# Kernel optimization log

Hardware: AMD Instinct MI355X
Metric: run time of the kernel (lower is better)

## Reference

```python
import jax, jax.numpy as jnp
import numpy as np

N = 50000      # nodes
E = 800000     # edges (no self loops; GATConv adds them itself)
F_IN = 128     # in_channels
ED = 16        # edge_attr_dim
H1, C1 = 8, 8  # layer-1 heads/channels -> 64 concat
OUT = 128      # out_channels
G = 256        # graphs in batch
NEG_SLOPE = 0.2


def setup_inputs() -> dict:
    key = jax.random.key(0)
    ks = jax.random.split(key, 20)
    x = jax.random.normal(ks[0], (N, F_IN), jnp.float32)
    src = jax.random.randint(ks[1], (E,), 0, N, jnp.int32)
    off = jax.random.randint(ks[2], (E,), 1, N, jnp.int32)
    dst = ((src + off) % N).astype(jnp.int32)  # guaranteed no self loops
    edge_index = jnp.stack([src, dst])
    edge_attr = jax.random.normal(ks[3], (E, ED), jnp.float32)
    batch = jnp.sort(jax.random.randint(ks[4], (N,), 0, G, jnp.int32))
    def glorot(k, shape, fan_in):
        return jax.random.normal(k, shape, jnp.float32) / np.sqrt(fan_in)
    params = dict(
        W1=glorot(ks[5], (F_IN, H1 * C1), F_IN),
        att_src1=glorot(ks[6], (H1, C1), C1),
        att_dst1=glorot(ks[7], (H1, C1), C1),
        att_edge1=glorot(ks[8], (H1, C1), C1),
        We1=glorot(ks[9], (ED, H1 * C1), ED),
        b1=jnp.zeros((H1 * C1,), jnp.float32),
        W2=glorot(ks[10], (H1 * C1, OUT), H1 * C1),
        att_src2=glorot(ks[11], (1, OUT), OUT),
        att_dst2=glorot(ks[12], (1, OUT), OUT),
        att_edge2=glorot(ks[13], (1, OUT), OUT),
        We2=glorot(ks[14], (ED, OUT), ED),
        b2=jnp.zeros((OUT,), jnp.float32),
    )
    return dict(x=x, edge_index=edge_index, edge_attr=edge_attr, batch=batch, **params)


def _segment_softmax(a, seg, n):
    m = jax.ops.segment_max(a, seg, num_segments=n)
    e = jnp.exp(a - m[seg])
    s = jax.ops.segment_sum(e, seg, num_segments=n)
    return e / (s[seg] + 1e-16)


def _gat_layer(x, src, dst, ea_full, W, a_s, a_d, a_e, We, b, heads, ch, concat):
    n = x.shape[0]
    xw = (x @ W).reshape(n, heads, ch)                       # [N,H,C]
    al_s = jnp.einsum('nhc,hc->nh', xw, a_s)                  # [N,H]
    al_d = jnp.einsum('nhc,hc->nh', xw, a_d)
    ew = (ea_full @ We).reshape(-1, heads, ch)                # [E',H,C]
    al_e = jnp.einsum('ehc,hc->eh', ew, a_e)
    alpha = al_s[src] + al_d[dst] + al_e                      # [E',H]
    alpha = jax.nn.leaky_relu(alpha, NEG_SLOPE)
    alpha = _segment_softmax(alpha, dst, n)                   # softmax over incoming edges
    out = jax.ops.segment_sum(xw[src] * alpha[:, :, None], dst, num_segments=n)
    out = out.reshape(n, heads * ch) if concat else out.mean(axis=1)
    return out + b


def reference(x, edge_index, edge_attr, batch,
              W1, att_src1, att_dst1, att_edge1, We1, b1,
              W2, att_src2, att_dst2, att_edge2, We2, b2):
    src, dst = edge_index[0], edge_index[1]
    n = x.shape[0]
    # add self loops; self-loop edge_attr = mean of incoming edge_attr (fill_value='mean')
    ones = jnp.ones((src.shape[0],), x.dtype)
    deg = jax.ops.segment_sum(ones, dst, num_segments=n)
    ea_self = jax.ops.segment_sum(edge_attr, dst, num_segments=n) / jnp.maximum(deg, 1.0)[:, None]
    loop = jnp.arange(n, dtype=src.dtype)
    src_f = jnp.concatenate([src, loop])
    dst_f = jnp.concatenate([dst, loop])
    ea_full = jnp.concatenate([edge_attr, ea_self], axis=0)

    h = _gat_layer(x, src_f, dst_f, ea_full, W1, att_src1, att_dst1, att_edge1, We1, b1, H1, C1, True)
    h = jax.nn.elu(h)
    h = _gat_layer(h, src_f, dst_f, ea_full, W2, att_src2, att_dst2, att_edge2, We2, b2, 1, OUT, True)

    # global mean pool over graphs
    cnt = jax.ops.segment_sum(jnp.ones((n,), h.dtype), batch, num_segments=G)
    pooled = jax.ops.segment_sum(h, batch, num_segments=G) / jnp.maximum(cnt, 1.0)[:, None]
    return pooled
```

## Files before the change

### kernel.cpp

```cpp
#include <hip/hip_runtime.h>
#include <hip/hip_bf16.h>
#include <math.h>

#define N_NODES 50000
#define N_EDGES 800000
#define F_IN    128
#define ED_DIM  16
#define D1      64
#define NGRAPH  256
#define OUT_C   128

__global__ void prep_kernel(const float* __restrict__ W1, const float* __restrict__ W2,
                            float* __restrict__ W1t, float* __restrict__ W2t) {
  int t = blockIdx.x * 256 + threadIdx.x;
  if (t < 64 * 128) {
    int k = t >> 6, c = t & 63;
    W1t[c * 128 + k] = W1[t];
    int k2 = t >> 7, c2 = t & 127;
    W2t[c2 * 64 + k2] = W2[t];
  }
}

__global__ void hist_kernel(const int* __restrict__ dst, int* __restrict__ deg) {
  int i = blockIdx.x * blockDim.x + threadIdx.x;
  int stride = gridDim.x * blockDim.x;
  for (; i < N_EDGES; i += stride) atomicAdd(&deg[dst[i]], 1);
}

__global__ void scan1_kernel(const int* __restrict__ deg, int* __restrict__ offs,
                             int* __restrict__ bsum) {
  __shared__ int sh[256];
  int b = blockIdx.x, t = threadIdx.x, i = b * 256 + t;
  int v = (i < N_NODES) ? deg[i] : 0;
  sh[t] = v;
  __syncthreads();
  for (int o = 1; o < 256; o <<= 1) {
    int tv = (t >= o) ? sh[t - o] : 0;
    __syncthreads();
    sh[t] += tv;
    __syncthreads();
  }
  if (i < N_NODES) offs[i + 1] = sh[t];
  if (t == 255) bsum[b] = sh[255];
}

__global__ void scan2_kernel(int* __restrict__ bsum) {
  __shared__ int sh[256];
  int t = threadIdx.x;
  sh[t] = (t < 196) ? bsum[t] : 0;
  __syncthreads();
  for (int o = 1; o < 256; o <<= 1) {
    int tv = (t >= o) ? sh[t - o] : 0;
    __syncthreads();
    sh[t] += tv;
    __syncthreads();
  }
  if (t < 196) bsum[t] = (t > 0) ? sh[t - 1] : 0;
}

__global__ void scan3_kernel(const int* __restrict__ bsum, int* __restrict__ offs) {
  int b = blockIdx.x, t = threadIdx.x, i = b * 256 + t;
  if (i < N_NODES) offs[i + 1] += bsum[b];
  if (i == 0) offs[0] = 0;
}

__global__ void scatter_kernel(const int* __restrict__ src, const int* __restrict__ dst,
                               const float* __restrict__ ea,
                               const float* __restrict__ We1, const float* __restrict__ ae1,
                               const float* __restrict__ We2, const float* __restrict__ ae2,
                               const int* __restrict__ offs, int* __restrict__ cnt,
                               int* __restrict__ csr_src,
                               float* __restrict__ al_e1s, float* __restrict__ al_e2s) {
  __shared__ float M1s[16][8];
  __shared__ float M2s[16];
  int t = threadIdx.x;
  if (t < 128) {
    int d = t >> 3, h = t & 7;
    float s = 0.f;
    #pragma unroll
    for (int c = 0; c < 8; ++c) s = fmaf(We1[d * 64 + h * 8 + c], ae1[h * 8 + c], s);
    M1s[d][h] = s;
  } else if (t < 144) {
    int d = t - 128;
    float s = 0.f;
    for (int c = 0; c < 128; ++c) s = fmaf(We2[d * 128 + c], ae2[c], s);
    M2s[d] = s;
  }
  __syncthreads();
  int i = blockIdx.x * blockDim.x + t;
  int stride = gridDim.x * blockDim.x;
  for (; i < N_EDGES; i += stride) {
    int s = src[i], d = dst[i];
    float e[16];
    const float4* ea4 = (const float4*)(ea + (size_t)i * 16);
    #pragma unroll
    for (int q = 0; q < 4; ++q) {
      float4 v = ea4[q];
      e[q * 4] = v.x; e[q * 4 + 1] = v.y; e[q * 4 + 2] = v.z; e[q * 4 + 3] = v.w;
    }
    int pos = offs[d] + atomicAdd(&cnt[d], 1);
    csr_src[pos] = s;
    float r[8];
    #pragma unroll
    for (int h = 0; h < 8; ++h) {
      float sacc = 0.f;
      #pragma unroll
      for (int dd = 0; dd < 16; ++dd) sacc = fmaf(e[dd], M1s[dd][h], sacc);
      r[h] = sacc;
    }
    float4* o4 = (float4*)(al_e1s + (size_t)pos * 8);
    o4[0] = make_float4(r[0], r[1], r[2], r[3]);
    o4[1] = make_float4(r[4], r[5], r[6], r[7]);
    float s2 = 0.f;
    #pragma unroll
    for (int dd = 0; dd < 16; ++dd) s2 = fmaf(e[dd], M2s[dd], s2);
    al_e2s[pos] = s2;
  }
}

__global__ __launch_bounds__(256) void gemm1_kernel(
    const float* __restrict__ x, const float* __restrict__ W1t,
    const float* __restrict__ as1, const float* __restrict__ ad1,
    float* __restrict__ xw1, float* __restrict__ al_s1, float* __restrict__ al_d1) {
  __shared__ float xl[64 * 132];
  __shared__ float wl[64 * 132];
  int t = threadIdx.x;
  int row0 = blockIdx.x * 64;
  const float4* xg = (const float4*)(x + (size_t)row0 * 128);
  const float4* wg = (const float4*)W1t;
  #pragma unroll
  for (int j = 0; j < 8; ++j) {
    int idx = t + j * 256;
    int r = idx >> 5, kq = idx & 31;
    float4 v = make_float4(0.f, 0.f, 0.f, 0.f);
    if (row0 + r < N_NODES) v = xg[r * 32 + kq];
    *(float4*)&xl[r * 132 + kq * 4] = v;
    *(float4*)&wl[(idx >> 5) * 132 + kq * 4] = wg[idx];
  }
  __syncthreads();
  int c0 = t & 15;
  int r4 = (t >> 4) * 4;
  float acc[4][4];
  #pragma unroll
  for (int i = 0; i < 4; ++i)
    #pragma unroll
    for (int j = 0; j < 4; ++j) acc[i][j] = 0.f;
  #pragma unroll 4
  for (int kq = 0; kq < 32; ++kq) {
    float4 xv[4], wv[4];
    #pragma unroll
    for (int i = 0; i < 4; ++i) xv[i] = *(const float4*)&xl[(r4 + i) * 132 + kq * 4];
    #pragma unroll
    for (int j = 0; j < 4; ++j) wv[j] = *(const float4*)&wl[(c0 + 16 * j) * 132 + kq * 4];
    #pragma unroll
    for (int i = 0; i < 4; ++i)
      #pragma unroll
      for (int j = 0; j < 4; ++j) {
        acc[i][j] = fmaf(xv[i].x, wv[j].x, acc[i][j]);
        acc[i][j] = fmaf(xv[i].y, wv[j].y, acc[i][j]);
        acc[i][j] = fmaf(xv[i].z, wv[j].z, acc[i][j]);
        acc[i][j] = fmaf(xv[i].w, wv[j].w, acc[i][j]);
      }
  }
  #pragma unroll
  for (int i = 0; i < 4; ++i) {
    int r = row0 + r4 + i;
    if (r < N_NODES) {
      #pragma unroll
      for (int j = 0; j < 4; ++j) xw1[(size_t)r * 64 + c0 + 16 * j] = acc[i][j];
    }
  }
  float ps[4][4], pd[4][4];
  #pragma unroll
  for (int j = 0; j < 4; ++j) {
    float asv = as1[c0 + 16 * j], adv = ad1[c0 + 16 * j];
    #pragma unroll
    for (int i = 0; i < 4; ++i) { ps[i][j] = acc[i][j] * asv; pd[i][j] = acc[i][j] * adv; }
  }
  #pragma unroll
  for (int m = 1; m <= 4; m <<= 1)
    #pragma unroll
    for (int i = 0; i < 4; ++i)
      #pragma unroll
      for (int j = 0; j < 4; ++j) {
        ps[i][j] += __shfl_xor(ps[i][j], m);
        pd[i][j] += __shfl_xor(pd[i][j], m);
      }
  if ((t & 7) == 0) {
    int half = (c0 >> 3) & 1;
    #pragma unroll
    for (int i = 0; i < 4; ++i) {
      int r = row0 + r4 + i;
      if (r < N_NODES) {
        #pragma unroll
        for (int j = 0; j < 4; ++j) {
          int h = 2 * j + half;
          al_s1[r * 8 + h] = ps[i][j];
          al_d1[r * 8 + h] = pd[i][j];
        }
      }
    }
  }
}

__global__ void agg1_kernel(const int* __restrict__ offs, const int* __restrict__ csr_src,
                            const float* __restrict__ al_s1, const float* __restrict__ al_d1,
                            const float* __restrict__ al_e1s, const float* __restrict__ xw1,
                            const float* __restrict__ b1, float* __restrict__ h1) {
  int node = blockIdx.x * 4 + (threadIdx.x >> 6);
  if (node >= N_NODES) return;
  int lane = threadIdx.x & 63;
  int h = lane >> 3;
  int base = offs[node], end = offs[node + 1];
  int degn = end - base;
  float adv = al_d1[node * 8 + h];
  float m = -INFINITY, ssum = 0.f, acc = 0.f, sume = 0.f;
  for (int j = base; j < end; ++j) {
    int sid = csr_src[j];
    float ae = al_e1s[(size_t)j * 8 + h];
    sume += ae;
    float a = al_s1[sid * 8 + h] + adv + ae;
    a = (a > 0.f) ? a : 0.2f * a;
    float nm = fmaxf(m, a);
    float sc = __expf(m - nm);
    float e = __expf(a - nm);
    ssum = ssum * sc + e;
    acc = acc * sc + e * xw1[(size_t)sid * 64 + lane];
    m = nm;
  }
  float aes = sume / (float)max(degn, 1);
  float a = al_s1[node * 8 + h] + adv + aes;
  a = (a > 0.f) ? a : 0.2f * a;
  float nm = fmaxf(m, a);
  float sc = __expf(m - nm);
  float e = __expf(a - nm);
  ssum = ssum * sc + e;
  acc = acc * sc + e * xw1[(size_t)node * 64 + lane];
  float o = acc / (ssum + 1e-16f) + b1[lane];
  h1[(size_t)node * 64 + lane] = (o > 0.f) ? o : expm1f(o);
}

__global__ __launch_bounds__(256) void gemm2_kernel(
    const float* __restrict__ h1, const float* __restrict__ W2t,
    const float* __restrict__ as2, const float* __restrict__ ad2,
    float* __restrict__ xw2, float* __restrict__ al_s2, float* __restrict__ al_d2) {
  __shared__ float hl[64 * 68];
  __shared__ float wl[128 * 68];
  int t = threadIdx.x;
  int row0 = blockIdx.x * 64;
  const float4* hg = (const float4*)(h1 + (size_t)row0 * 64);
  const float4* wg = (const float4*)W2t;
  #pragma unroll
  for (int j = 0; j < 4; ++j) {
    int idx = t + j * 256;
    int r = idx >> 4, kq = idx & 15;
    float4 v = make_float4(0.f, 0.f, 0.f, 0.f);
    if (row0 + r < N_NODES) v = hg[r * 16 + kq];
    *(float4*)&hl[r * 68 + kq * 4] = v;
  }
  #pragma unroll
  for (int j = 0; j < 8; ++j) {
    int idx = t + j * 256;
    int c = idx >> 4, kq = idx & 15;
    *(float4*)&wl[c * 68 + kq * 4] = wg[idx];
  }
  __syncthreads();
  int c0 = t & 31;
  int r8 = (t >> 5) * 8;
  float acc[8][4];
  #pragma unroll
  for (int i = 0; i < 8; ++i)
    #pragma unroll
    for (int j = 0; j < 4; ++j) acc[i][j] = 0.f;
  #pragma unroll 2
  for (int kq = 0; kq < 16; ++kq) {
    float4 xv[8], wv[4];
    #pragma unroll
    for (int i = 0; i < 8; ++i) xv[i] = *(const float4*)&hl[(r8 + i) * 68 + kq * 4];
    #pragma unroll
    for (int j = 0; j < 4; ++j) wv[j] = *(const float4*)&wl[(c0 + 32 * j) * 68 + kq * 4];
    #pragma unroll
    for (int i = 0; i < 8; ++i)
      #pragma unroll
      for (int j = 0; j < 4; ++j) {
        acc[i][j] = fmaf(xv[i].x, wv[j].x, acc[i][j]);
        acc[i][j] = fmaf(xv[i].y, wv[j].y, acc[i][j]);
        acc[i][j] = fmaf(xv[i].z, wv[j].z, acc[i][j]);
        acc[i][j] = fmaf(xv[i].w, wv[j].w, acc[i][j]);
      }
  }
  #pragma unroll
  for (int i = 0; i < 8; ++i) {
    int r = row0 + r8 + i;
    if (r < N_NODES) {
      #pragma unroll
      for (int j = 0; j < 4; ++j) xw2[(size_t)r * 128 + c0 + 32 * j] = acc[i][j];
    }
  }
  float ps[8], pd[8];
  #pragma unroll
  for (int i = 0; i < 8; ++i) { ps[i] = 0.f; pd[i] = 0.f; }
  #pragma unroll
  for (int j = 0; j < 4; ++j) {
    float asv = as2[c0 + 32 * j], adv = ad2[c0 + 32 * j];
    #pragma unroll
    for (int i = 0; i < 8; ++i) { ps[i] = fmaf(acc[i][j], asv, ps[i]); pd[i] = fmaf(acc[i][j], adv, pd[i]); }
  }
  #pragma unroll
  for (int m = 1; m <= 16; m <<= 1)
    #pragma unroll
    for (int i = 0; i < 8; ++i) {
      ps[i] += __shfl_xor(ps[i], m);
      pd[i] += __shfl_xor(pd[i], m);
    }
  if (c0 == 0) {
    #pragma unroll
    for (int i = 0; i < 8; ++i) {
      int r = row0 + r8 + i;
      if (r < N_NODES) { al_s2[r] = ps[i]; al_d2[r] = pd[i]; }
    }
  }
}

__global__ void agg2_kernel(const int* __restrict__ offs, const int* __restrict__ csr_src,
                            const float* __restrict__ al_s2, const float* __restrict__ al_d2,
                            const float* __restrict__ al_e2s, const float* __restrict__ xw2,
                            const float* __restrict__ b2, float* __restrict__ h2) {
  int node = blockIdx.x * 4 + (threadIdx.x >> 6);
  if (node >= N_NODES) return;
  int lane = threadIdx.x & 63;
  int base = offs[node], end = offs[node + 1];
  int degn = end - base;
  float adv = al_d2[node];
  float m = -INFINITY, ssum = 0.f, acc0 = 0.f, acc1 = 0.f, sume = 0.f;
  for (int j = base; j < end; ++j) {
    int sid = csr_src[j];
    float ae = al_e2s[j];
    sume += ae;
    float a = al_s2[sid] + adv + ae;
    a = (a > 0.f) ? a : 0.2f * a;
    float nm = fmaxf(m, a);
    float sc = __expf(m - nm);
    float e = __expf(a - nm);
    ssum = ssum * sc + e;
    acc0 = acc0 * sc + e * xw2[(size_t)sid * 128 + lane];
    acc1 = acc1 * sc + e * xw2[(size_t)sid * 128 + 64 + lane];
    m = nm;
  }
  float aes = sume / (float)max(degn, 1);
  float a = al_s2[node] + adv + aes;
  a = (a > 0.f) ? a : 0.2f * a;
  float nm = fmaxf(m, a);
  float sc = __expf(m - nm);
  float e = __expf(a - nm);
  ssum = ssum * sc + e;
  acc0 = acc0 * sc + e * xw2[(size_t)node * 128 + lane];
  acc1 = acc1 * sc + e * xw2[(size_t)node * 128 + 64 + lane];
  float inv = 1.f / (ssum + 1e-16f);
  h2[(size_t)node * 128 + lane] = acc0 * inv + b2[lane];
  h2[(size_t)node * 128 + 64 + lane] = acc1 * inv + b2[lane + 64];
}

__global__ void gstart_kernel(const int* __restrict__ batch, int* __restrict__ gstart) {
  int n = blockIdx.x * blockDim.x + threadIdx.x;
  if (n >= N_NODES) return;
  int b = batch[n];
  if (n == 0) {
    for (int g = 0; g <= b; ++g) gstart[g] = 0;
  } else {
    int pb = batch[n - 1];
    for (int g = pb + 1; g <= b; ++g) gstart[g] = n;
  }
  if (n == N_NODES - 1) {
    for (int g = b + 1; g <= NGRAPH; ++g) gstart[g] = N_NODES;
  }
}

__global__ void pool_kernel(const float* __restrict__ h2, const int* __restrict__ gstart,
                            float* __restrict__ out) {
  int g = blockIdx.x;
  int c = threadIdx.x;
  int s0 = gstart[g], s1 = gstart[g + 1];
  float s = 0.f;
  for (int r = s0; r < s1; ++r) s += h2[(size_t)r * 128 + c];
  out[g * 128 + c] = s / fmaxf((float)(s1 - s0), 1.f);
}

extern "C" void kernel_launch(void* const* d_in, const int* in_sizes, int n_in,
                              void* d_out, int out_size, void* d_ws, size_t ws_size,
                              hipStream_t stream) {
  const float* x      = (const float*)d_in[0];
  const int*   eidx   = (const int*)d_in[1];
  const float* ea     = (const float*)d_in[2];
  const int*   batch  = (const int*)d_in[3];
  const float* W1     = (const float*)d_in[4];
  const float* as1    = (const float*)d_in[5];
  const float* ad1    = (const float*)d_in[6];
  const float* ae1    = (const float*)d_in[7];
  const float* We1    = (const float*)d_in[8];
  const float* b1     = (const float*)d_in[9];
  const float* W2     = (const float*)d_in[10];
  const float* as2    = (const float*)d_in[11];
  const float* ad2    = (const float*)d_in[12];
  const float* ae2    = (const float*)d_in[13];
  const float* We2    = (const float*)d_in[14];
  const float* b2     = (const float*)d_in[15];
  float* out = (float*)d_out;

  const int* src = eidx;
  const int* dst = eidx + N_EDGES;

  char* base = (char*)d_ws;
  size_t o = 0;
  #define ALLOC(name, bytes) size_t name = o; o += (((size_t)(bytes)) + 255) & ~(size_t)255;
  ALLOC(o_degcnt, 2 * N_NODES * 4)
  ALLOC(o_offs,   (N_NODES + 1) * 4)
  ALLOC(o_bsum,   256 * 4)
  ALLOC(o_csr,    N_EDGES * 4)
  ALLOC(o_ale1,   (size_t)N_EDGES * 8 * 4)
  ALLOC(o_ale2,   N_EDGES * 4)
  ALLOC(o_w1t,    64 * 128 * 4)
  ALLOC(o_w2t,    128 * 64 * 4)
  ALLOC(o_xw1,    (size_t)N_NODES * 64 * 4)
  ALLOC(o_als1,   N_NODES * 8 * 4)
  ALLOC(o_ald1,   N_NODES * 8 * 4)
  ALLOC(o_h1,     (size_t)N_NODES * 64 * 4)
  ALLOC(o_xw2,    (size_t)N_NODES * 128 * 4)
  ALLOC(o_als2,   N_NODES * 4)
  ALLOC(o_ald2,   N_NODES * 4)
  ALLOC(o_h2,     (size_t)N_NODES * 128 * 4)
  ALLOC(o_gs,     (NGRAPH + 1) * 4)
  #undef ALLOC

  int*   deg     = (int*)(base + o_degcnt);
  int*   cnt     = deg + N_NODES;
  int*   offs    = (int*)(base + o_offs);
  int*   bsum    = (int*)(base + o_bsum);
  int*   csr_src = (int*)(base + o_csr);
  float* al_e1s  = (float*)(base + o_ale1);
  float* al_e2s  = (float*)(base + o_ale2);
  float* W1t     = (float*)(base + o_w1t);
  float* W2t     = (float*)(base + o_w2t);
  float* xw1     = (float*)(base + o_xw1);
  float* al_s1   = (float*)(base + o_als1);
  float* al_d1   = (float*)(base + o_ald1);
  float* h1      = (float*)(base + o_h1);
  float* xw2     = (float*)(base + o_xw2);
  float* al_s2   = (float*)(base + o_als2);
  float* al_d2   = (float*)(base + o_ald2);
  float* h2      = (float*)(base + o_h2);
  int*   gstart  = (int*)(base + o_gs);

  hipMemsetAsync(deg, 0, (size_t)2 * N_NODES * 4, stream);

  prep_kernel<<<32, 256, 0, stream>>>(W1, W2, W1t, W2t);
  hist_kernel<<<1024, 256, 0, stream>>>(dst, deg);
  scan1_kernel<<<196, 256, 0, stream>>>(deg, offs, bsum);
  scan2_kernel<<<1, 256, 0, stream>>>(bsum);
  scan3_kernel<<<196, 256, 0, stream>>>(bsum, offs);
  scatter_kernel<<<2048, 256, 0, stream>>>(src, dst, ea, We1, ae1, We2, ae2,
                                           offs, cnt, csr_src, al_e1s, al_e2s);
  gemm1_kernel<<<(N_NODES + 63) / 64, 256, 0, stream>>>(x, W1t, as1, ad1, xw1, al_s1, al_d1);
  agg1_kernel<<<(N_NODES + 3) / 4, 256, 0, stream>>>(offs, csr_src, al_s1, al_d1,
                                                     al_e1s, xw1, b1, h1);
  gemm2_kernel<<<(N_NODES + 63) / 64, 256, 0, stream>>>(h1, W2t, as2, ad2, xw2, al_s2, al_d2);
  agg2_kernel<<<(N_NODES + 3) / 4, 256, 0, stream>>>(offs, csr_src, al_s2, al_d2,
                                                     al_e2s, xw2, b2, h2);
  gstart_kernel<<<(N_NODES + 255) / 256, 256, 0, stream>>>(batch, gstart);
  pool_kernel<<<NGRAPH, 128, 0, stream>>>(h2, gstart, out);
}
```

Baseline: 587.0 us.

## Pack per-edge CSR records and unroll aggregation loops by two

Merges the CSR source index, the eight layer-1 edge attention logits and the layer-2 edge logit into one 64-byte record per edge, so each aggregation step reads a single cache line instead of three separate arrays. Both aggregation kernels now process two edges per iteration, so the gathers for both edges are issued before the online-softmax update, which adds memory-level parallelism. The h2 buffer now aliases xw1, which is dead by that point, shrinking the workspace. The cost is a larger scatter write: 64 bytes per edge, including padding zeros, versus 40 bytes before.

```diff
diff --git a/kernel.cpp b/kernel.cpp
--- a/kernel.cpp
+++ b/kernel.cpp
@@ -69,8 +69,7 @@
                                const float* __restrict__ We1, const float* __restrict__ ae1,
                                const float* __restrict__ We2, const float* __restrict__ ae2,
                                const int* __restrict__ offs, int* __restrict__ cnt,
-                               int* __restrict__ csr_src,
-                               float* __restrict__ al_e1s, float* __restrict__ al_e2s) {
+                               float* __restrict__ rec) {
   __shared__ float M1s[16][8];
   __shared__ float M2s[16];
   int t = threadIdx.x;
@@ -99,7 +98,6 @@
       e[q * 4] = v.x; e[q * 4 + 1] = v.y; e[q * 4 + 2] = v.z; e[q * 4 + 3] = v.w;
     }
     int pos = offs[d] + atomicAdd(&cnt[d], 1);
-    csr_src[pos] = s;
     float r[8];
     #pragma unroll
     for (int h = 0; h < 8; ++h) {
@@ -108,13 +106,14 @@
       for (int dd = 0; dd < 16; ++dd) sacc = fmaf(e[dd], M1s[dd][h], sacc);
       r[h] = sacc;
     }
-    float4* o4 = (float4*)(al_e1s + (size_t)pos * 8);
-    o4[0] = make_float4(r[0], r[1], r[2], r[3]);
-    o4[1] = make_float4(r[4], r[5], r[6], r[7]);
     float s2 = 0.f;
     #pragma unroll
     for (int dd = 0; dd < 16; ++dd) s2 = fmaf(e[dd], M2s[dd], s2);
-    al_e2s[pos] = s2;
+    float4* o4 = (float4*)(rec + (size_t)pos * 16);
+    o4[0] = make_float4(__int_as_float(s), r[0], r[1], r[2]);
+    o4[1] = make_float4(r[3], r[4], r[5], r[6]);
+    o4[2] = make_float4(r[7], s2, 0.f, 0.f);
+    o4[3] = make_float4(0.f, 0.f, 0.f, 0.f);
   }
 }
 
@@ -203,9 +202,9 @@
   }
 }
 
-__global__ void agg1_kernel(const int* __restrict__ offs, const int* __restrict__ csr_src,
+__global__ void agg1_kernel(const int* __restrict__ offs, const float* __restrict__ rec,
                             const float* __restrict__ al_s1, const float* __restrict__ al_d1,
-                            const float* __restrict__ al_e1s, const float* __restrict__ xw1,
+                            const float* __restrict__ xw1,
                             const float* __restrict__ b1, float* __restrict__ h1) {
   int node = blockIdx.x * 4 + (threadIdx.x >> 6);
   if (node >= N_NODES) return;
@@ -215,17 +214,36 @@
   int degn = end - base;
   float adv = al_d1[node * 8 + h];
   float m = -INFINITY, ssum = 0.f, acc = 0.f, sume = 0.f;
-  for (int j = base; j < end; ++j) {
-    int sid = csr_src[j];
-    float ae = al_e1s[(size_t)j * 8 + h];
-    sume += ae;
-    float a = al_s1[sid * 8 + h] + adv + ae;
-    a = (a > 0.f) ? a : 0.2f * a;
-    float nm = fmaxf(m, a);
-    float sc = __expf(m - nm);
-    float e = __expf(a - nm);
-    ssum = ssum * sc + e;
-    acc = acc * sc + e * xw1[(size_t)sid * 64 + lane];
+  int j = base;
+  for (; j + 1 < end; j += 2) {
+    const float* r0 = rec + (size_t)j * 16;
+    const float* r1 = r0 + 16;
+    int s0 = __float_as_int(r0[0]); float ae0 = r0[1 + h];
+    int s1 = __float_as_int(r1[0]); float ae1 = r1[1 + h];
+    float x0 = xw1[(size_t)s0 * 64 + lane];
+    float x1 = xw1[(size_t)s1 * 64 + lane];
+    float a0 = al_s1[s0 * 8 + h] + adv + ae0;
+    float a1 = al_s1[s1 * 8 + h] + adv + ae1;
+    sume += ae0 + ae1;
+    a0 = (a0 > 0.f) ? a0 : 0.2f * a0;
+    a1 = (a1 > 0.f) ? a1 : 0.2f * a1;
+    float nm = fmaxf(m, fmaxf(a0, a1));
+    float sc = __expf(m - nm), e0 = __expf(a0 - nm), e1 = __expf(a1 - nm);
+    ssum = ssum * sc + e0 + e1;
+    acc = acc * sc + e0 * x0 + e1 * x1;
+    m = nm;
+  }
+  if (j < end) {
+    const float* r0 = rec + (size_t)j * 16;
+    int s0 = __float_as_int(r0[0]); float ae0 = r0[1 + h];
+    float x0 = xw1[(size_t)s0 * 64 + lane];
+    float a0 = al_s1[s0 * 8 + h] + adv + ae0;
+    sume += ae0;
+    a0 = (a0 > 0.f) ? a0 : 0.2f * a0;
+    float nm = fmaxf(m, a0);
+    float sc = __expf(m - nm), e0 = __expf(a0 - nm);
+    ssum = ssum * sc + e0;
+    acc = acc * sc + e0 * x0;
     m = nm;
   }
   float aes = sume / (float)max(degn, 1);
@@ -322,9 +340,9 @@
   }
 }
 
-__global__ void agg2_kernel(const int* __restrict__ offs, const int* __restrict__ csr_src,
+__global__ void agg2_kernel(const int* __restrict__ offs, const float* __restrict__ rec,
                             const float* __restrict__ al_s2, const float* __restrict__ al_d2,
-                            const float* __restrict__ al_e2s, const float* __restrict__ xw2,
+                            const float* __restrict__ xw2,
                             const float* __restrict__ b2, float* __restrict__ h2) {
   int node = blockIdx.x * 4 + (threadIdx.x >> 6);
   if (node >= N_NODES) return;
@@ -333,18 +351,41 @@
   int degn = end - base;
   float adv = al_d2[node];
   float m = -INFINITY, ssum = 0.f, acc0 = 0.f, acc1 = 0.f, sume = 0.f;
-  for (int j = base; j < end; ++j) {
-    int sid = csr_src[j];
-    float ae = al_e2s[j];
-    sume += ae;
-    float a = al_s2[sid] + adv + ae;
-    a = (a > 0.f) ? a : 0.2f * a;
-    float nm = fmaxf(m, a);
-    float sc = __expf(m - nm);
-    float e = __expf(a - nm);
-    ssum = ssum * sc + e;
-    acc0 = acc0 * sc + e * xw2[(size_t)sid * 128 + lane];
-    acc1 = acc1 * sc + e * xw2[(size_t)sid * 128 + 64 + lane];
+  int j = base;
+  for (; j + 1 < end; j += 2) {
+    const float* r0 = rec + (size_t)j * 16;
+    const float* r1 = r0 + 16;
+    int s0 = __float_as_int(r0[0]); float ae0 = r0[9];
+    int s1 = __float_as_int(r1[0]); float ae1 = r1[9];
+    float x0a = xw2[(size_t)s0 * 128 + lane];
+    float x0b = xw2[(size_t)s0 * 128 + 64 + lane];
+    float x1a = xw2[(size_t)s1 * 128 + lane];
+    float x1b = xw2[(size_t)s1 * 128 + 64 + lane];
+    float a0 = al_s2[s0] + adv + ae0;
+    float a1 = al_s2[s1] + adv + ae1;
+    sume += ae0 + ae1;
+    a0 = (a0 > 0.f) ? a0 : 0.2f * a0;
+    a1 = (a1 > 0.f) ? a1 : 0.2f * a1;
+    float nm = fmaxf(m, fmaxf(a0, a1));
+    float sc = __expf(m - nm), e0 = __expf(a0 - nm), e1 = __expf(a1 - nm);
+    ssum = ssum * sc + e0 + e1;
+    acc0 = acc0 * sc + e0 * x0a + e1 * x1a;
+    acc1 = acc1 * sc + e0 * x0b + e1 * x1b;
+    m = nm;
+  }
+  if (j < end) {
+    const float* r0 = rec + (size_t)j * 16;
+    int s0 = __float_as_int(r0[0]); float ae0 = r0[9];
+    float x0a = xw2[(size_t)s0 * 128 + lane];
+    float x0b = xw2[(size_t)s0 * 128 + 64 + lane];
+    float a0 = al_s2[s0] + adv + ae0;
+    sume += ae0;
+    a0 = (a0 > 0.f) ? a0 : 0.2f * a0;
+    float nm = fmaxf(m, a0);
+    float sc = __expf(m - nm), e0 = __expf(a0 - nm);
+    ssum = ssum * sc + e0;
+    acc0 = acc0 * sc + e0 * x0a;
+    acc1 = acc1 * sc + e0 * x0b;
     m = nm;
   }
   float aes = sume / (float)max(degn, 1);
@@ -416,9 +457,7 @@
   ALLOC(o_degcnt, 2 * N_NODES * 4)
   ALLOC(o_offs,   (N_NODES + 1) * 4)
   ALLOC(o_bsum,   256 * 4)
-  ALLOC(o_csr,    N_EDGES * 4)
-  ALLOC(o_ale1,   (size_t)N_EDGES * 8 * 4)
-  ALLOC(o_ale2,   N_EDGES * 4)
+  ALLOC(o_rec,    (size_t)N_EDGES * 16 * 4)
   ALLOC(o_w1t,    64 * 128 * 4)
   ALLOC(o_w2t,    128 * 64 * 4)
   ALLOC(o_xw1,    (size_t)N_NODES * 64 * 4)
@@ -428,7 +467,6 @@
   ALLOC(o_xw2,    (size_t)N_NODES * 128 * 4)
   ALLOC(o_als2,   N_NODES * 4)
   ALLOC(o_ald2,   N_NODES * 4)
-  ALLOC(o_h2,     (size_t)N_NODES * 128 * 4)
   ALLOC(o_gs,     (NGRAPH + 1) * 4)
   #undef ALLOC
 
@@ -436,9 +474,7 @@
   int*   cnt     = deg + N_NODES;
   int*   offs    = (int*)(base + o_offs);
   int*   bsum    = (int*)(base + o_bsum);
-  int*   csr_src = (int*)(base + o_csr);
-  float* al_e1s  = (float*)(base + o_ale1);
-  float* al_e2s  = (float*)(base + o_ale2);
+  float* rec     = (float*)(base + o_rec);
   float* W1t     = (float*)(base + o_w1t);
   float* W2t     = (float*)(base + o_w2t);
   float* xw1     = (float*)(base + o_xw1);
@@ -448,7 +484,7 @@
   float* xw2     = (float*)(base + o_xw2);
   float* al_s2   = (float*)(base + o_als2);
   float* al_d2   = (float*)(base + o_ald2);
-  float* h2      = (float*)(base + o_h2);
+  float* h2      = (float*)(base + o_xw1);
   int*   gstart  = (int*)(base + o_gs);
 
   hipMemsetAsync(deg, 0, (size_t)2 * N_NODES * 4, stream);
@@ -459,13 +495,11 @@
   scan2_kernel<<<1, 256, 0, stream>>>(bsum);
   scan3_kernel<<<196, 256, 0, stream>>>(bsum, offs);
   scatter_kernel<<<2048, 256, 0, stream>>>(src, dst, ea, We1, ae1, We2, ae2,
-                                           offs, cnt, csr_src, al_e1s, al_e2s);
+                                           offs, cnt, rec);
   gemm1_kernel<<<(N_NODES + 63) / 64, 256, 0, stream>>>(x, W1t, as1, ad1, xw1, al_s1, al_d1);
-  agg1_kernel<<<(N_NODES + 3) / 4, 256, 0, stream>>>(offs, csr_src, al_s1, al_d1,
-                                                     al_e1s, xw1, b1, h1);
+  agg1_kernel<<<(N_NODES + 3) / 4, 256, 0, stream>>>(offs, rec, al_s1, al_d1, xw1, b1, h1);
   gemm2_kernel<<<(N_NODES + 63) / 64, 256, 0, stream>>>(h1, W2t, as2, ad2, xw2, al_s2, al_d2);
-  agg2_kernel<<<(N_NODES + 3) / 4, 256, 0, stream>>>(offs, csr_src, al_s2, al_d2,
-                                                     al_e2s, xw2, b2, h2);
+  agg2_kernel<<<(N_NODES + 3) / 4, 256, 0, stream>>>(offs, rec, al_s2, al_d2, xw2, b2, h2);
   gstart_kernel<<<(N_NODES + 255) / 256, 256, 0, stream>>>(batch, gstart);
   pool_kernel<<<NGRAPH, 128, 0, stream>>>(h2, gstart, out);
 }
```

Measured after the change: 512.9 us. -12.6%, faster.
